# Optimization experiments

Hardware: AMD Instinct MI355X
Metric: run time of the kernel (lower is better)

## Reference

```python
import jax, jax.numpy as jnp
import numpy as np

B = 2048; SQ = 64; PC = 24; F = 16; H = 128; D = 256; T = 128; A = 4672
NSQ = B * SQ; NPC = B * PC


def setup_inputs() -> dict:
    key = jax.random.key(0)
    ks = iter(jax.random.split(key, 48))
    def nrm(shape, s=0.05):
        return jax.random.normal(next(ks), shape, dtype=jnp.float32) * s
    def edges(e_per, src_per, dst_per):
        # per-graph local edges: graph_offset + local node index
        g = jnp.repeat(jnp.arange(B), e_per)
        src = g * src_per + jax.random.randint(next(ks), (B * e_per,), 0, src_per)
        dst = g * dst_per + jax.random.randint(next(ks), (B * e_per,), 0, dst_per)
        return jnp.stack([src, dst]).astype(jnp.int32)
    gp = jnp.repeat(jnp.arange(B), PC)
    occ_src = jnp.arange(NPC, dtype=jnp.int32)                       # each piece occupies one square
    occ_dst = (gp * SQ + jax.random.randint(next(ks), (NPC,), 0, SQ)).astype(jnp.int32)
    ei_occ = jnp.stack([occ_src, occ_dst])                           # piece -> square
    ei_rev = ei_occ[::-1]                                            # square -> piece (rev_occupied_by)
    return dict(
        x_sq=jax.random.normal(next(ks), (NSQ, F), dtype=jnp.float32),
        x_pc=jax.random.normal(next(ks), (NPC, F), dtype=jnp.float32),
        W_in_sq=nrm((F, H)), b_in_sq=jnp.zeros((H,), jnp.float32),
        W_in_pc=nrm((F, H)), b_in_pc=jnp.zeros((H,), jnp.float32),
        W_adj=nrm((H, H)), W_occ=nrm((H, H)), W_att=nrm((H, H)), W_def=nrm((H, H)), W_rev=nrm((H, H)),
        W_out=nrm((H, D)), b_out=jnp.zeros((D,), jnp.float32),
        W_pt=nrm((D, T)), b_pt=jnp.zeros((T,), jnp.float32),
        W_vt=nrm((D, T)), b_vt=jnp.zeros((T,), jnp.float32),
        W_ph=nrm((T, A)), b_ph=jnp.zeros((A,), jnp.float32),
        W_vh=nrm((T, 1)), b_vh=jnp.zeros((1,), jnp.float32),
        ei_adj=edges(420, SQ, SQ),
        ei_occ=ei_occ,
        ei_att=edges(40, PC, PC),
        ei_def=edges(40, PC, PC),
        ei_rev=ei_rev,
        square_batch=jnp.repeat(jnp.arange(B), SQ).astype(jnp.int32),
        piece_batch=gp.astype(jnp.int32),
    )


def reference(x_sq, x_pc, W_in_sq, b_in_sq, W_in_pc, b_in_pc,
              W_adj, W_occ, W_att, W_def, W_rev, W_out, b_out,
              W_pt, b_pt, W_vt, b_vt, W_ph, b_ph, W_vh, b_vh,
              ei_adj, ei_occ, ei_att, ei_def, ei_rev, square_batch, piece_batch):
    gelu = jax.nn.gelu
    seg = jax.ops.segment_sum
    # per-node-type input encoders
    h_sq = gelu(x_sq @ W_in_sq + b_in_sq)          # [NSQ, H]
    h_pc = gelu(x_pc @ W_in_pc + b_in_pc)          # [NPC, H]
    # heterogeneous message passing: gather -> linear -> scatter-sum per edge type
    agg_sq = seg(h_sq[ei_adj[0]] @ W_adj, ei_adj[1], NSQ)
    agg_sq = agg_sq + seg(h_pc[ei_occ[0]] @ W_occ, ei_occ[1], NSQ)
    agg_pc = seg(h_pc[ei_att[0]] @ W_att, ei_att[1], NPC)
    agg_pc = agg_pc + seg(h_pc[ei_def[0]] @ W_def, ei_def[1], NPC)
    agg_pc = agg_pc + seg(h_sq[ei_rev[0]] @ W_rev, ei_rev[1], NPC)
    h_sq2 = gelu(h_sq + agg_sq)
    h_pc2 = gelu(h_pc + agg_pc)
    # project to embed_dim and mean-pool per graph
    out_sq = gelu(h_sq2 @ W_out + b_out)           # [NSQ, D]
    out_pc = gelu(h_pc2 @ W_out + b_out)           # [NPC, D]
    shared = seg(out_sq, square_batch, B) / SQ + seg(out_pc, piece_batch, B) / PC  # [B, D]
    # dual trunks + heads (exactly as in ChessNetwork.forward)
    policy_logits = gelu(shared @ W_pt + b_pt) @ W_ph + b_ph        # [B, 4672]
    value = jnp.tanh(gelu(shared @ W_vt + b_vt) @ W_vh + b_vh)      # [B, 1]
    return policy_logits, value
```

## Files before the change

kernel.cpp:

```cpp
#include <hip/hip_runtime.h>

#define BATCH 2048
#define SQN 64
#define PCN 24
#define FEAT 16
#define HID 128
#define DOUT 256
#define TDIM 128
#define ADIM 4672
#define NSQT (BATCH*SQN)
#define NPCT (BATCH*PCN)
#define E_ADJ 420
#define E_ATT 40
#define E_ADJ_TOT (BATCH*E_ADJ)
#define E_ATT_TOT (BATCH*E_ATT)

typedef unsigned short u16;
typedef unsigned int u32;
typedef __attribute__((ext_vector_type(8))) short bf16x8;
typedef __attribute__((ext_vector_type(8))) unsigned short u16x8;
typedef __attribute__((ext_vector_type(4))) float f32x4;
typedef __attribute__((ext_vector_type(2))) unsigned int u32x2;
typedef __attribute__((ext_vector_type(4))) unsigned int u32x4;

#define OFF_WADJ_H 0
#define OFF_WADJ_L 16384
#define OFF_WOCC_H 32768
#define OFF_WOCC_L 49152
#define OFF_WATT_H 65536
#define OFF_WATT_L 81920
#define OFF_WDEF_H 98304
#define OFF_WDEF_L 114688
#define OFF_WREV_H 131072
#define OFF_WREV_L 147456
#define OFF_WOUT_H 163840
#define OFF_WOUT_L 196608
#define OFF_WPH_H  229376
#define OFF_WPH_L  827392
#define OFF_WINSQ_H 1425408
#define OFF_WINSQ_L 1429504
#define OFF_WINPC_H 1433600
#define OFF_WINPC_L 1437696
#define WB_TOTAL    1441792

#define K_SMEM 81920

#define PHP_OFF  0
#define PAH_OFF  24576
#define PAL_OFF  36864
#define PEA_OFF  49152
#define PED_OFF  49472
#define PSA_OFF  49792
#define PSD_OFF  50112
#define PRSA_OFF 50432
#define PCUA_OFF 50692
#define PCNA_OFF 50948
#define PRSD_OFF 51204
#define PCUD_OFF 51464
#define PCND_OFF 51720
#define PRVS_OFF 51976
#define PRVD_OFF 52168

__device__ __forceinline__ u32 cvtpk(float a, float b) {
    u32 r;
    asm("v_cvt_pk_bf16_f32 %0, %1, %2" : "=v"(r) : "v"(a), "v"(b));
    return r;
}
__device__ __forceinline__ u16 f2b(float x) { return (u16)cvtpk(x, x); }
__device__ __forceinline__ float b2f(u16 h) { return __uint_as_float(((u32)h) << 16); }
__device__ __forceinline__ void split2(float x, u16& h, u16& l) {
    u32 wp = cvtpk(x, x);
    h = (u16)wp;
    float r = x - __uint_as_float(wp << 16);
    l = (u16)cvtpk(r, r);
}
__device__ __forceinline__ void split_pk(float a, float b, u32& wh, u32& wl) {
    wh = cvtpk(a, b);
    float ra = a - __uint_as_float(wh << 16);
    float rb = b - __uint_as_float(wh & 0xffff0000u);
    wl = cvtpk(ra, rb);
}
__device__ __forceinline__ float gelu_f(float x) {
    float x2 = x * x;
    float z2 = x * __builtin_fmaf(x2, 0.0713548162f, 1.5957691216f);
    float e = __expf(z2);
    return x - x * __fdividef(1.0f, e + 1.0f);
}
__device__ __forceinline__ f32x4 MFMA(bf16x8 a, bf16x8 b, f32x4 c) {
    return __builtin_amdgcn_mfma_f32_16x16x32_bf16(a, b, c, 0, 0, 0);
}
__device__ __forceinline__ bf16x8 bzero() {
    bf16x8 v = {0,0,0,0,0,0,0,0}; return v;
}
__device__ __forceinline__ void xfrag(const float* __restrict__ xrow, int g,
                                      bf16x8& ah, bf16x8& al)
{
    const f32x4 a = *(const f32x4*)(xrow + g*8);
    const f32x4 b = *(const f32x4*)(xrow + g*8 + 4);
    u32 h0,h1,h2,h3,l0,l1,l2,l3;
    split_pk(a[0], a[1], h0, l0);
    split_pk(a[2], a[3], h1, l1);
    split_pk(b[0], b[1], h2, l2);
    split_pk(b[2], b[3], h3, l3);
    u32x4 vh = {h0,h1,h2,h3};
    u32x4 vl = {l0,l1,l2,l3};
    ah = *(bf16x8*)&vh;
    al = *(bf16x8*)&vl;
}

template<int NT, int RT>
__device__ __forceinline__ void gemm_nt(
    const unsigned char* Ah, const unsigned char* Al,
    const u16* __restrict__ wh, const u16* __restrict__ wl,
    int ntBase, int lane, int g, int lr, f32x4 (&c)[NT][RT])
{
    const int sw = lr << 4;
    #pragma unroll
    for (int ks = 0; ks < 4; ++ks) {
        const int ko = ks*64 + g*16;
        bf16x8 ah[RT], al[RT];
        #pragma unroll
        for (int rt = 0; rt < RT; ++rt) {
            const int ro = (rt*16 + lr)*256 + (ko ^ sw);
            ah[rt] = *(const bf16x8*)(Ah + ro);
            al[rt] = *(const bf16x8*)(Al + ro);
        }
        #pragma unroll
        for (int ntl = 0; ntl < NT; ++ntl) {
            bf16x8 bh = *(const bf16x8*)(wh + (((ntBase+ntl)*4 + ks)*64 + lane)*8);
            bf16x8 bl = *(const bf16x8*)(wl + (((ntBase+ntl)*4 + ks)*64 + lane)*8);
            #pragma unroll
            for (int rt = 0; rt < RT; ++rt) {
                c[ntl][rt] = MFMA(ah[rt], bh, c[ntl][rt]);
                c[ntl][rt] = MFMA(al[rt], bh, c[ntl][rt]);
                c[ntl][rt] = MFMA(ah[rt], bl, c[ntl][rt]);
            }
        }
    }
}

__device__ __forceinline__ void gather_f32_8(
    const unsigned char* H, const int* srt, int st, int en, int cq8, float (&acc)[16])
{
    for (int i = st; i < en; ++i) {
        const int s = srt[i];
        const unsigned char* rp = H + s*512;
        const int sw2 = (s & 15) << 4;
        #pragma unroll
        for (int u = 0; u < 4; ++u) {
            f32x4 v = *(const f32x4*)(rp + ((cq8*64 + u*16) ^ sw2));
            acc[u*4+0] += v[0]; acc[u*4+1] += v[1];
            acc[u*4+2] += v[2]; acc[u*4+3] += v[3];
        }
    }
}
__device__ __forceinline__ void writeA_8(
    unsigned char* Ah, unsigned char* Al, int d, int cq8, const float (&acc)[16])
{
    unsigned char* wh = Ah + d*256;
    unsigned char* wl = Al + d*256;
    const int dw = (d & 15) << 4;
    #pragma unroll
    for (int u = 0; u < 2; ++u) {
        u32 oh[4], ol[4];
        #pragma unroll
        for (int j = 0; j < 4; ++j)
            split_pk(acc[u*8 + j*2], acc[u*8 + j*2 + 1], oh[j], ol[j]);
        u32x4 vh = {oh[0], oh[1], oh[2], oh[3]};
        u32x4 vl = {ol[0], ol[1], ol[2], ol[3]};
        *(u32x4*)(wh + ((cq8*32 + u*16) ^ dw)) = vh;
        *(u32x4*)(wl + ((cq8*32 + u*16) ^ dw)) = vl;
    }
}

__global__ __launch_bounds__(256) void k_prep(
    const float* __restrict__ W_adj, const float* __restrict__ W_occ,
    const float* __restrict__ W_att, const float* __restrict__ W_def,
    const float* __restrict__ W_rev, const float* __restrict__ W_out,
    const float* __restrict__ W_ph,
    const float* __restrict__ W_in_sq, const float* __restrict__ W_in_pc,
    u16* __restrict__ wb)
{
    int gid = blockIdx.x*256 + threadIdx.x;
    int fid = gid >> 6, lane = gid & 63;
    int g8 = (lane >> 4) * 8, lr = lane & 15;
    u16x8 vh, vl;
    if (fid >= 1392) {
        int f = fid - 1392;
        const float* src = (f < 8) ? W_in_sq : W_in_pc;
        int oh = (f < 8) ? OFF_WINSQ_H : OFF_WINPC_H;
        int ol = (f < 8) ? OFF_WINSQ_L : OFF_WINPC_L;
        int nt = f & 7;
        int col = nt*16 + lr;
        #pragma unroll
        for (int j = 0; j < 8; ++j) {
            int k = g8 + j;
            float v = (k < 16) ? src[k*HID + col] : 0.f;
            u16 h, l; split2(v, h, l);
            vh[j] = h; vl[j] = l;
        }
        *(u16x8*)(wb + oh + (nt*64 + lane)*8) = vh;
        *(u16x8*)(wb + ol + (nt*64 + lane)*8) = vl;
        return;
    }
    const float* src; int ld, f, oh, ol;
    if (fid < 32)       { src = W_adj; ld = HID;  f = fid;      oh = OFF_WADJ_H; ol = OFF_WADJ_L; }
    else if (fid < 64)  { src = W_occ; ld = HID;  f = fid-32;   oh = OFF_WOCC_H; ol = OFF_WOCC_L; }
    else if (fid < 96)  { src = W_att; ld = HID;  f = fid-64;   oh = OFF_WATT_H; ol = OFF_WATT_L; }
    else if (fid < 128) { src = W_def; ld = HID;  f = fid-96;   oh = OFF_WDEF_H; ol = OFF_WDEF_L; }
    else if (fid < 160) { src = W_rev; ld = HID;  f = fid-128;  oh = OFF_WREV_H; ol = OFF_WREV_L; }
    else if (fid < 224) { src = W_out; ld = DOUT; f = fid-160;  oh = OFF_WOUT_H; ol = OFF_WOUT_L; }
    else                { src = W_ph;  ld = ADIM; f = fid-224;  oh = OFF_WPH_H;  ol = OFF_WPH_L; }
    int nt = f >> 2, kb = f & 3;
    int col = nt*16 + lr;
    #pragma unroll
    for (int j = 0; j < 8; ++j) {
        int k = kb*32 + g8 + j;
        u16 h, l; split2(src[k*ld + col], h, l);
        vh[j] = h; vl[j] = l;
    }
    *(u16x8*)(wb + oh + (f*64 + lane)*8) = vh;
    *(u16x8*)(wb + ol + (f*64 + lane)*8) = vl;
}

__device__ __forceinline__ void sq_path(
    unsigned char* SMb, int b, int t,
    const float* __restrict__ x_sq, const float* __restrict__ x_pc,
    const float* __restrict__ b_in_sq, const float* __restrict__ b_in_pc,
    const float* __restrict__ b_out,
    const int* __restrict__ ei_adj, const int* __restrict__ ei_occ,
    const u16* __restrict__ wb, float* __restrict__ shared_sq)
{
    unsigned char* Hs_h  = SMb;
    unsigned char* Hs_l  = SMb + 16384;
    int*           Mint  = (int*)(SMb + 32768);
    unsigned char* HOT_h = SMb + 32768;
    unsigned char* HOT_l = SMb + 40960;
    unsigned char* Mocc  = SMb + 49152;
    unsigned char* A_h   = SMb + 32768;
    unsigned char* A_l   = SMb + 49152;
    unsigned char* Madj  = SMb + 65536;
    unsigned char* Hp    = SMb + 73728;

    const int w = t >> 6, lane = t & 63, g = lane >> 4, lr = lane & 15;
    const int colp = w*16 + lr;

    #pragma unroll
    for (int i = 0; i < 8; ++i) Mint[t + i*512] = 0;
    ((u32*)Mocc)[t] = 0;
    ((u32*)Mocc)[t + 512] = 0;
    ((u32*)(Hp + 6144))[t] = 0;
    __syncthreads();

    for (int i = t; i < E_ADJ; i += 512) {
        int s = ei_adj[b*E_ADJ + i] - b*SQN;
        int d = ei_adj[E_ADJ_TOT + b*E_ADJ + i] - b*SQN;
        atomicAdd(&Mint[d*64 + s], 1);
    }
    if (t < PCN) {
        int p = ei_occ[b*PCN + t] - b*PCN;
        int d = ei_occ[NPCT + b*PCN + t] - b*SQN;
        *(u16*)(Mocc + d*64 + ((p*2) ^ ((d&3)<<4))) = 0x3F80;
    }
    __syncthreads();

    #pragma unroll
    for (int ii = 0; ii < 4; ++ii) {
        int i = t + ii*512;
        int row = i >> 5, cp = i & 31;
        float v0 = (float)Mint[row*64 + cp*2];
        float v1 = (float)Mint[row*64 + cp*2 + 1];
        *(u32*)(Madj + row*128 + ((cp*4) ^ ((row&7)<<4))) = cvtpk(v0, v1);
    }
    float hv[16];
    {
        const f32x4 z = {0.f,0.f,0.f,0.f};
        f32x4 ch[4] = {z,z,z,z};
        {
            bf16x8 bh = *(const bf16x8*)(wb + OFF_WINSQ_H + (w*64 + lane)*8);
            bf16x8 bl = *(const bf16x8*)(wb + OFF_WINSQ_L + (w*64 + lane)*8);
            #pragma unroll
            for (int rt = 0; rt < 4; ++rt) {
                bf16x8 ah = bzero(), al = bzero();
                if (g < 2) xfrag(x_sq + (b*SQN + rt*16 + lr)*FEAT, g, ah, al);
                ch[rt] = MFMA(ah, bh, ch[rt]);
                ch[rt] = MFMA(al, bh, ch[rt]);
                ch[rt] = MFMA(ah, bl, ch[rt]);
            }
        }
        const float bbs = b_in_sq[colp];
        #pragma unroll
        for (int rt = 0; rt < 4; ++rt)
            #pragma unroll
            for (int r = 0; r < 4; ++r) {
                const int row = rt*16 + g*4 + r;
                float h = gelu_f(ch[rt][r] + bbs);
                hv[rt*4 + r] = h;
                u16 hh, ll; split2(h, hh, ll);
                const int bo = row*256 + ((colp*2) ^ ((row&15)<<4));
                *(u16*)(Hs_h + bo) = hh;
                *(u16*)(Hs_l + bo) = ll;
            }
        f32x4 cp2[2] = {z, z};
        {
            bf16x8 bh = *(const bf16x8*)(wb + OFF_WINPC_H + (w*64 + lane)*8);
            bf16x8 bl = *(const bf16x8*)(wb + OFF_WINPC_L + (w*64 + lane)*8);
            #pragma unroll
            for (int rt = 0; rt < 2; ++rt) {
                const int row = rt*16 + lr;
                bf16x8 ah = bzero(), al = bzero();
                if (g < 2 && row < PCN) xfrag(x_pc + (b*PCN + row)*FEAT, g, ah, al);
                cp2[rt] = MFMA(ah, bh, cp2[rt]);
                cp2[rt] = MFMA(al, bh, cp2[rt]);
                cp2[rt] = MFMA(ah, bl, cp2[rt]);
            }
        }
        const float bbp = b_in_pc[colp];
        #pragma unroll
        for (int rt = 0; rt < 2; ++rt)
            #pragma unroll
            for (int r = 0; r < 4; ++r) {
                const int row = rt*16 + g*4 + r;
                if (row < PCN) {
                    float h = gelu_f(cp2[rt][r] + bbp);
                    *(u16*)(Hp + row*256 + ((colp*2) ^ ((row&15)<<4))) = f2b(h);
                }
            }
    }
    __syncthreads();

    f32x4 hwj[4], hwo[2];
    {
        const f32x4 z = {0.f,0.f,0.f,0.f};
        hwj[0]=z; hwj[1]=z; hwj[2]=z; hwj[3]=z; hwo[0]=z; hwo[1]=z;
        const int sw15 = lr << 4;
        #pragma unroll
        for (int ks = 0; ks < 4; ++ks) {
            const int ko = ks*64 + g*16;
            bf16x8 bh = *(const bf16x8*)(wb + OFF_WADJ_H + ((w*4 + ks)*64 + lane)*8);
            bf16x8 bl = *(const bf16x8*)(wb + OFF_WADJ_L + ((w*4 + ks)*64 + lane)*8);
            #pragma unroll
            for (int rt = 0; rt < 4; ++rt) {
                const int ro = (rt*16 + lr)*256 + (ko ^ sw15);
                bf16x8 ah = *(const bf16x8*)(Hs_h + ro);
                bf16x8 al = *(const bf16x8*)(Hs_l + ro);
                hwj[rt] = MFMA(ah, bh, hwj[rt]);
                hwj[rt] = MFMA(al, bh, hwj[rt]);
                hwj[rt] = MFMA(ah, bl, hwj[rt]);
            }
            bf16x8 oh = *(const bf16x8*)(wb + OFF_WOCC_H + ((w*4 + ks)*64 + lane)*8);
            bf16x8 ol = *(const bf16x8*)(wb + OFF_WOCC_L + ((w*4 + ks)*64 + lane)*8);
            #pragma unroll
            for (int rt = 0; rt < 2; ++rt) {
                const int ro = (rt*16 + lr)*256 + (ko ^ sw15);
                bf16x8 ah = *(const bf16x8*)(Hp + ro);
                hwo[rt] = MFMA(ah, oh, hwo[rt]);
                hwo[rt] = MFMA(ah, ol, hwo[rt]);
            }
        }
    }
    __syncthreads();

    {
        const int swj = (lr & 7) << 4;
        #pragma unroll
        for (int rt = 0; rt < 4; ++rt) {
            u32 h01, l01, h23, l23;
            split_pk(hwj[rt][0], hwj[rt][1], h01, l01);
            split_pk(hwj[rt][2], hwj[rt][3], h23, l23);
            const int off = colp*128 + ((rt*32 + g*8) ^ swj);
            *(u32x2*)(Hs_h + off) = (u32x2){h01, h23};
            *(u32x2*)(Hs_l + off) = (u32x2){l01, l23};
        }
        const int swo = (lr & 3) << 4;
        #pragma unroll
        for (int rt = 0; rt < 2; ++rt) {
            u32 h01, l01, h23, l23;
            split_pk(hwo[rt][0], hwo[rt][1], h01, l01);
            split_pk(hwo[rt][2], hwo[rt][3], h23, l23);
            const int off = colp*64 + ((rt*32 + g*8) ^ swo);
            *(u32x2*)(HOT_h + off) = (u32x2){h01, h23};
            *(u32x2*)(HOT_l + off) = (u32x2){l01, l23};
        }
    }
    __syncthreads();

    f32x4 c1[4];
    {
        const f32x4 z = {0.f,0.f,0.f,0.f};
        c1[0]=z; c1[1]=z; c1[2]=z; c1[3]=z;
        const int swj = (lr & 7) << 4;
        #pragma unroll
        for (int ks = 0; ks < 2; ++ks) {
            const int bo = colp*128 + ((ks*64 + g*16) ^ swj);
            bf16x8 bh = *(const bf16x8*)(Hs_h + bo);
            bf16x8 bl = *(const bf16x8*)(Hs_l + bo);
            #pragma unroll
            for (int rt = 0; rt < 4; ++rt) {
                const int ao = (rt*16 + lr)*128 + ((ks*64 + g*16) ^ swj);
                bf16x8 am = *(const bf16x8*)(Madj + ao);
                c1[rt] = MFMA(am, bh, c1[rt]);
                c1[rt] = MFMA(am, bl, c1[rt]);
            }
        }
        const int swo = (lr & 3) << 4;
        {
            const int bo = colp*64 + ((g*16) ^ swo);
            bf16x8 bh = *(const bf16x8*)(HOT_h + bo);
            bf16x8 bl = *(const bf16x8*)(HOT_l + bo);
            #pragma unroll
            for (int rt = 0; rt < 4; ++rt) {
                const int ao = (rt*16 + lr)*64 + ((g*16) ^ swo);
                bf16x8 am = *(const bf16x8*)(Mocc + ao);
                c1[rt] = MFMA(am, bh, c1[rt]);
                c1[rt] = MFMA(am, bl, c1[rt]);
            }
        }
    }
    __syncthreads();

    #pragma unroll
    for (int rt = 0; rt < 4; ++rt)
        #pragma unroll
        for (int r = 0; r < 4; ++r) {
            const int row = rt*16 + g*4 + r;
            float h2 = gelu_f(c1[rt][r] + hv[rt*4 + r]);
            u16 hh, ll; split2(h2, hh, ll);
            const int bo = row*256 + ((colp*2) ^ ((row&15)<<4));
            *(u16*)(A_h + bo) = hh;
            *(u16*)(A_l + bo) = ll;
        }
    __syncthreads();

    f32x4 c2[2][4];
    {
        const f32x4 z = {0.f,0.f,0.f,0.f};
        #pragma unroll
        for (int n = 0; n < 2; ++n)
            #pragma unroll
            for (int rt = 0; rt < 4; ++rt) c2[n][rt] = z;
    }
    gemm_nt<2,4>(A_h, A_l, wb + OFF_WOUT_H, wb + OFF_WOUT_L, w*2, lane, g, lr, c2);
    #pragma unroll
    for (int ntl = 0; ntl < 2; ++ntl) {
        const int col = (w*2 + ntl)*16 + lr;
        const float bias = b_out[col];
        float cs = 0.f;
        #pragma unroll
        for (int rt = 0; rt < 4; ++rt)
            #pragma unroll
            for (int r = 0; r < 4; ++r) cs += gelu_f(c2[ntl][rt][r] + bias);
        cs += __shfl_xor(cs, 16);
        cs += __shfl_xor(cs, 32);
        if (lane < 16) shared_sq[b*DOUT + col] = cs * (1.0f/64.0f);
    }
}

__device__ __forceinline__ void pc_path(
    unsigned char* SMb, int pcb, int t,
    const float* __restrict__ x_sq, const float* __restrict__ x_pc,
    const float* __restrict__ b_in_sq, const float* __restrict__ b_in_pc,
    const float* __restrict__ b_out,
    const int* __restrict__ ei_att, const int* __restrict__ ei_def,
    const int* __restrict__ ei_rev,
    const u16* __restrict__ wb, float* __restrict__ shared_pc)
{
    unsigned char* Hp = SMb + PHP_OFF;
    unsigned char* Ah = SMb + PAH_OFF;
    unsigned char* Al = SMb + PAL_OFF;
    int* ea_pk = (int*)(SMb + PEA_OFF);
    int* ed_pk = (int*)(SMb + PED_OFF);
    int* srt_a = (int*)(SMb + PSA_OFF);
    int* srt_d = (int*)(SMb + PSD_OFF);
    int* rs_a  = (int*)(SMb + PRSA_OFF);
    int* cur_a = (int*)(SMb + PCUA_OFF);
    int* cnt_a = (int*)(SMb + PCNA_OFF);
    int* rs_d  = (int*)(SMb + PRSD_OFF);
    int* cur_d = (int*)(SMb + PCUD_OFF);
    int* cnt_d = (int*)(SMb + PCND_OFF);
    int* rv_s  = (int*)(SMb + PRVS_OFF);
    int* rv_d  = (int*)(SMb + PRVD_OFF);

    const int w = t >> 6, lane = t & 63, g = lane >> 4, lr = lane & 15;
    const int NR = 2*PCN;

    for (int i = t; i < 2*E_ATT; i += 512) {
        int sb = (i >= E_ATT) ? 1 : 0;
        int e = i - sb*E_ATT;
        int gb = pcb*2 + sb;
        int ro = sb*PCN - gb*PCN;
        int s = ei_att[gb*E_ATT + e] + ro;
        int d = ei_att[E_ATT_TOT + gb*E_ATT + e] + ro;
        ea_pk[i] = s | (d << 16);
        s = ei_def[gb*E_ATT + e] + ro;
        d = ei_def[E_ATT_TOT + gb*E_ATT + e] + ro;
        ed_pk[i] = s | (d << 16);
    }
    if (t < NR) {
        int sb = (t >= PCN) ? 1 : 0;
        int gb = pcb*2 + sb;
        int p = t - sb*PCN;
        rv_s[t] = ei_rev[gb*PCN + p];
        rv_d[t] = ei_rev[NPCT + gb*PCN + p] - gb*PCN + sb*PCN;
    }
    if (t < 64) { cnt_a[t] = 0; cnt_d[t] = 0; }
    __syncthreads();

    for (int i = t; i < 2*E_ATT; i += 512) {
        atomicAdd(&cnt_a[ea_pk[i] >> 16], 1);
        atomicAdd(&cnt_d[ed_pk[i] >> 16], 1);
    }
    __syncthreads();

    if (t < 64) {
        int v = cnt_a[t], o0 = v;
        for (int o = 1; o < 64; o <<= 1) { int u = __shfl_up(v, o); if (t >= o) v += u; }
        rs_a[t+1] = v; cur_a[t] = v - o0; if (t == 0) rs_a[0] = 0;
    } else if (t < 128) {
        int l = t - 64;
        int v = cnt_d[l], o0 = v;
        for (int o = 1; o < 64; o <<= 1) { int u = __shfl_up(v, o); if (l >= o) v += u; }
        rs_d[l+1] = v; cur_d[l] = v - o0; if (l == 0) rs_d[0] = 0;
    }
    __syncthreads();

    for (int i = t; i < 2*E_ATT; i += 512) {
        int pk = ea_pk[i];
        int p = atomicAdd(&cur_a[pk >> 16], 1); srt_a[p] = pk & 0xffff;
        pk = ed_pk[i];
        p = atomicAdd(&cur_d[pk >> 16], 1); srt_d[p] = pk & 0xffff;
    }
    {
        const int colp = w*16 + lr;
        const f32x4 z = {0.f,0.f,0.f,0.f};
        f32x4 cp[3] = {z,z,z};
        {
            bf16x8 bh = *(const bf16x8*)(wb + OFF_WINPC_H + (w*64 + lane)*8);
            bf16x8 bl = *(const bf16x8*)(wb + OFF_WINPC_L + (w*64 + lane)*8);
            #pragma unroll
            for (int rt = 0; rt < 3; ++rt) {
                bf16x8 ah = bzero(), al = bzero();
                if (g < 2) xfrag(x_pc + (pcb*NR + rt*16 + lr)*FEAT, g, ah, al);
                cp[rt] = MFMA(ah, bh, cp[rt]);
                cp[rt] = MFMA(al, bh, cp[rt]);
                cp[rt] = MFMA(ah, bl, cp[rt]);
            }
        }
        const float bbp = b_in_pc[colp];
        #pragma unroll
        for (int rt = 0; rt < 3; ++rt)
            #pragma unroll
            for (int r = 0; r < 4; ++r) {
                const int row = rt*16 + g*4 + r;
                float h = gelu_f(cp[rt][r] + bbp);
                *(float*)(Hp + row*512 + ((colp*4) ^ ((row&15)<<4))) = h;
            }
        f32x4 cr[3] = {z,z,z};
        {
            bf16x8 bh = *(const bf16x8*)(wb + OFF_WINSQ_H + (w*64 + lane)*8);
            bf16x8 bl = *(const bf16x8*)(wb + OFF_WINSQ_L + (w*64 + lane)*8);
            #pragma unroll
            for (int rt = 0; rt < 3; ++rt) {
                bf16x8 ah = bzero(), al = bzero();
                if (g < 2) {
                    int gr = rv_s[rt*16 + lr];
                    xfrag(x_sq + gr*FEAT, g, ah, al);
                }
                cr[rt] = MFMA(ah, bh, cr[rt]);
                cr[rt] = MFMA(al, bh, cr[rt]);
                cr[rt] = MFMA(ah, bl, cr[rt]);
            }
        }
        const float bbs = b_in_sq[colp];
        #pragma unroll
        for (int rt = 0; rt < 3; ++rt)
            #pragma unroll
            for (int r = 0; r < 4; ++r) {
                const int row0 = rt*16 + g*4 + r;
                const int dr = rv_d[row0];
                float h = gelu_f(cr[rt][r] + bbs);
                u16 hh, ll; split2(h, hh, ll);
                const int bo = dr*256 + ((colp*2) ^ ((dr&15)<<4));
                *(u16*)(Ah + bo) = hh;
                *(u16*)(Al + bo) = ll;
            }
    }
    __syncthreads();

    f32x4 c1[1][3];
    {
        const f32x4 z = {0.f,0.f,0.f,0.f};
        #pragma unroll
        for (int rt = 0; rt < 3; ++rt) c1[0][rt] = z;
    }
    gemm_nt<1,3>(Ah, Al, wb + OFF_WREV_H, wb + OFF_WREV_L, w, lane, g, lr, c1);
    __syncthreads();

    {
        const int d = t >> 3, cq8 = t & 7;
        if (d < NR) {
            float acc[16];
            #pragma unroll
            for (int i = 0; i < 16; ++i) acc[i] = 0.f;
            gather_f32_8(Hp, srt_a, rs_a[d], rs_a[d+1], cq8, acc);
            writeA_8(Ah, Al, d, cq8, acc);
        }
    }
    __syncthreads();

    gemm_nt<1,3>(Ah, Al, wb + OFF_WATT_H, wb + OFF_WATT_L, w, lane, g, lr, c1);
    __syncthreads();

    {
        const int d = t >> 3, cq8 = t & 7;
        if (d < NR) {
            float acc[16];
            #pragma unroll
            for (int i = 0; i < 16; ++i) acc[i] = 0.f;
            gather_f32_8(Hp, srt_d, rs_d[d], rs_d[d+1], cq8, acc);
            writeA_8(Ah, Al, d, cq8, acc);
        }
    }
    __syncthreads();

    gemm_nt<1,3>(Ah, Al, wb + OFF_WDEF_H, wb + OFF_WDEF_L, w, lane, g, lr, c1);
    __syncthreads();

    {
        const int colp = w*16 + lr;
        #pragma unroll
        for (int rt = 0; rt < 3; ++rt)
            #pragma unroll
            for (int r = 0; r < 4; ++r) {
                const int row = rt*16 + g*4 + r;
                float hvv = *(const float*)(Hp + row*512 + ((colp*4) ^ ((row&15)<<4)));
                float h2 = gelu_f(c1[0][rt][r] + hvv);
                u16 hh, ll; split2(h2, hh, ll);
                const int bo = row*256 + ((colp*2) ^ ((row&15)<<4));
                *(u16*)(Ah + bo) = hh;
                *(u16*)(Al + bo) = ll;
            }
    }
    __syncthreads();

    f32x4 c2[2][3];
    {
        const f32x4 z = {0.f,0.f,0.f,0.f};
        #pragma unroll
        for (int n = 0; n < 2; ++n)
            #pragma unroll
            for (int rt = 0; rt < 3; ++rt) c2[n][rt] = z;
    }
    gemm_nt<2,3>(Ah, Al, wb + OFF_WOUT_H, wb + OFF_WOUT_L, w*2, lane, g, lr, c2);
    #pragma unroll
    for (int ntl = 0; ntl < 2; ++ntl) {
        const int col = (w*2 + ntl)*16 + lr;
        const float bias = b_out[col];
        float s0 = 0.f, s1 = 0.f;
        #pragma unroll
        for (int r = 0; r < 4; ++r) s0 += gelu_f(c2[ntl][0][r] + bias);
        {
            float tt = 0.f;
            #pragma unroll
            for (int r = 0; r < 4; ++r) tt += gelu_f(c2[ntl][1][r] + bias);
            s0 += (g < 2) ? tt : 0.f;
            s1 += (g < 2) ? 0.f : tt;
        }
        #pragma unroll
        for (int r = 0; r < 4; ++r) s1 += gelu_f(c2[ntl][2][r] + bias);
        s0 += __shfl_xor(s0, 16); s0 += __shfl_xor(s0, 32);
        s1 += __shfl_xor(s1, 16); s1 += __shfl_xor(s1, 32);
        if (lane < 16) {
            const int b0 = pcb*2, b1 = b0 + 1;
            shared_pc[b0*DOUT + col] = s0 * (1.0f/PCN);
            shared_pc[b1*DOUT + col] = s1 * (1.0f/PCN);
        }
    }
}

__global__ __launch_bounds__(512, 4) void k_main(
    const float* __restrict__ x_sq, const float* __restrict__ x_pc,
    const float* __restrict__ b_in_sq, const float* __restrict__ b_in_pc,
    const float* __restrict__ b_out,
    const int* __restrict__ ei_adj, const int* __restrict__ ei_occ,
    const int* __restrict__ ei_att, const int* __restrict__ ei_def,
    const int* __restrict__ ei_rev,
    const u16* __restrict__ wb,
    float* __restrict__ shared_sq, float* __restrict__ shared_pc)
{
    extern __shared__ __align__(16) unsigned char SMb[];
    const int bid = blockIdx.x;
    const int grp = bid / 3, rem = bid - grp*3;
    if (rem < 2) {
        sq_path(SMb, grp*2 + rem, threadIdx.x, x_sq, x_pc, b_in_sq, b_in_pc,
                b_out, ei_adj, ei_occ, wb, shared_sq);
    } else {
        pc_path(SMb, grp, threadIdx.x, x_sq, x_pc, b_in_sq, b_in_pc,
                b_out, ei_att, ei_def, ei_rev, wb, shared_pc);
    }
}

__global__ __launch_bounds__(256) void k_head(
    const float* __restrict__ shared_sq, const float* __restrict__ shared_pc,
    const float* __restrict__ W_pt, const float* __restrict__ b_pt,
    const float* __restrict__ W_vt, const float* __restrict__ b_vt,
    const float* __restrict__ W_vh, const float* __restrict__ b_vh,
    u16* __restrict__ tpol_h, u16* __restrict__ tpol_l, float* __restrict__ out_value)
{
    __shared__ float sh[2*DOUT];
    __shared__ float vred[2*TDIM];
    const int t = threadIdx.x;
    const int hh = t >> 7, j = t & 127;
    const int b = blockIdx.x*2 + hh;
    for (int i = t; i < 2*DOUT; i += 256)
        sh[i] = shared_sq[blockIdx.x*2*DOUT + i] + shared_pc[blockIdx.x*2*DOUT + i];
    __syncthreads();
    const float* s = sh + hh*DOUT;
    float ap = b_pt[j], av = b_vt[j];
    #pragma unroll 8
    for (int k = 0; k < DOUT; ++k) {
        float sv = s[k];
        ap += sv * W_pt[k*TDIM + j];
        av += sv * W_vt[k*TDIM + j];
    }
    float tv = gelu_f(ap);
    u16 th, tl; split2(tv, th, tl);
    tpol_h[b*TDIM + j] = th;
    tpol_l[b*TDIM + j] = tl;
    vred[hh*TDIM + j] = gelu_f(av) * W_vh[j];
    __syncthreads();
    for (int stp = 64; stp > 0; stp >>= 1) {
        if (j < stp) vred[hh*TDIM + j] += vred[hh*TDIM + j + stp];
        __syncthreads();
    }
    if (j == 0) out_value[b] = tanhf(vred[hh*TDIM] + b_vh[0]);
}

__global__ __launch_bounds__(256) void k_pol(
    const u16* __restrict__ tpol_h, const u16* __restrict__ tpol_l,
    const u16* __restrict__ wb, const float* __restrict__ b_ph,
    float* __restrict__ pol)
{
    const u16* wph_h = wb + OFF_WPH_H;
    const u16* wph_l = wb + OFF_WPH_L;
    const int t = threadIdx.x, w = t >> 6, lane = t & 63, g = lane >> 4, lr = lane & 15;
    const int nt = blockIdx.x*4 + w;
    const int rbase = blockIdx.y*64;
    f32x4 acc[4];
    const f32x4 z = {0.f,0.f,0.f,0.f};
    #pragma unroll
    for (int rt = 0; rt < 4; ++rt) acc[rt] = z;
    #pragma unroll
    for (int ks = 0; ks < 4; ++ks) {
        bf16x8 bh = *(const bf16x8*)(wph_h + ((nt*4 + ks)*64 + lane)*8);
        bf16x8 bl = *(const bf16x8*)(wph_l + ((nt*4 + ks)*64 + lane)*8);
        #pragma unroll
        for (int rt = 0; rt < 4; ++rt) {
            const int ro = (rbase + rt*16 + lr)*TDIM + ks*32 + g*8;
            bf16x8 ah = *(const bf16x8*)(tpol_h + ro);
            bf16x8 al = *(const bf16x8*)(tpol_l + ro);
            acc[rt] = MFMA(ah, bh, acc[rt]);
            acc[rt] = MFMA(al, bh, acc[rt]);
            acc[rt] = MFMA(ah, bl, acc[rt]);
        }
    }
    const float bias = b_ph[nt*16 + lr];
    #pragma unroll
    for (int rt = 0; rt < 4; ++rt)
        #pragma unroll
        for (int r = 0; r < 4; ++r) {
            int row = rbase + rt*16 + g*4 + r;
            pol[(size_t)row*ADIM + nt*16 + lr] = acc[rt][r] + bias;
        }
}

extern "C" void kernel_launch(void* const* d_in, const int* in_sizes, int n_in,
                              void* d_out, int out_size, void* d_ws, size_t ws_size,
                              hipStream_t stream) {
    (void)in_sizes; (void)n_in; (void)out_size; (void)ws_size;
    const float* x_sq    = (const float*)d_in[0];
    const float* x_pc    = (const float*)d_in[1];
    const float* W_in_sq = (const float*)d_in[2];
    const float* b_in_sq = (const float*)d_in[3];
    const float* W_in_pc = (const float*)d_in[4];
    const float* b_in_pc = (const float*)d_in[5];
    const float* W_adj   = (const float*)d_in[6];
    const float* W_occ   = (const float*)d_in[7];
    const float* W_att   = (const float*)d_in[8];
    const float* W_def   = (const float*)d_in[9];
    const float* W_rev   = (const float*)d_in[10];
    const float* W_out   = (const float*)d_in[11];
    const float* b_out   = (const float*)d_in[12];
    const float* W_pt    = (const float*)d_in[13];
    const float* b_pt    = (const float*)d_in[14];
    const float* W_vt    = (const float*)d_in[15];
    const float* b_vt    = (const float*)d_in[16];
    const float* W_ph    = (const float*)d_in[17];
    const float* b_ph    = (const float*)d_in[18];
    const float* W_vh    = (const float*)d_in[19];
    const float* b_vh    = (const float*)d_in[20];
    const int* ei_adj    = (const int*)d_in[21];
    const int* ei_occ    = (const int*)d_in[22];
    const int* ei_att    = (const int*)d_in[23];
    const int* ei_def    = (const int*)d_in[24];
    const int* ei_rev    = (const int*)d_in[25];

    float* out = (float*)d_out;
    float* pol = out;
    float* val = out + (size_t)BATCH * ADIM;

    float* shared_sq = (float*)d_ws;
    float* shared_pc = shared_sq + BATCH*DOUT;
    u16* tpol_h = (u16*)(shared_pc + BATCH*DOUT);
    u16* tpol_l = tpol_h + BATCH*TDIM;
    u16* wb     = tpol_l + BATCH*TDIM;

    hipFuncSetAttribute((const void*)k_main,
                        hipFuncAttributeMaxDynamicSharedMemorySize, K_SMEM);

    k_prep<<<352, 256, 0, stream>>>(W_adj, W_occ, W_att, W_def, W_rev, W_out, W_ph,
                                    W_in_sq, W_in_pc, wb);
    k_main<<<3072, 512, K_SMEM, stream>>>(x_sq, x_pc, b_in_sq, b_in_pc, b_out,
                                          ei_adj, ei_occ, ei_att, ei_def, ei_rev,
                                          wb, shared_sq, shared_pc);
    k_head<<<BATCH/2, 256, 0, stream>>>(shared_sq, shared_pc, W_pt, b_pt, W_vt, b_vt,
                                        W_vh, b_vh, tpol_h, tpol_l, val);
    k_pol<<<dim3(ADIM/64, BATCH/64), 256, 0, stream>>>(tpol_h, tpol_l, wb, b_ph, pol);
}
```

Measured before the change: 198.2 us.

## Move trunk head GEMMs onto MFMA with pre-split bf16 weights

The policy/value trunk projection (shared @ W_pt, shared @ W_vt) now runs on MFMA matrix cores using a three-term bf16 hi/lo split, with W_pt and W_vt pre-packed in k_prep. k_head switches from 1024 scalar-FMA blocks to 64 blocks of 512 threads, each covering 32 rows, and reduces the value head with wave shuffles. Separately, the A-fragment loads in gemm_nt are moved inside the inner loop to cut register pressure. The head now has few blocks, which may underuse the GPU, and the three-term split keeps precision close to fp32.

New measurement: 187.7 us. 1.06x faster.

```diff
diff --git a/kernel.cpp b/kernel.cpp
--- a/kernel.cpp
+++ b/kernel.cpp
@@ -41,7 +41,11 @@
 #define OFF_WINSQ_L 1429504
 #define OFF_WINPC_H 1433600
 #define OFF_WINPC_L 1437696
-#define WB_TOTAL    1441792
+#define OFF_WPT_H  1441792
+#define OFF_WPT_L  1474560
+#define OFF_WVT_H  1507328
+#define OFF_WVT_L  1540096
+#define WB_TOTAL   1572864
 
 #define K_SMEM 81920
 
@@ -117,23 +121,19 @@
     const int sw = lr << 4;
     #pragma unroll
     for (int ks = 0; ks < 4; ++ks) {
-        const int ko = ks*64 + g*16;
-        bf16x8 ah[RT], al[RT];
-        #pragma unroll
-        for (int rt = 0; rt < RT; ++rt) {
-            const int ro = (rt*16 + lr)*256 + (ko ^ sw);
-            ah[rt] = *(const bf16x8*)(Ah + ro);
-            al[rt] = *(const bf16x8*)(Al + ro);
-        }
+        const int ko = (ks*64 + g*16) ^ sw;
         #pragma unroll
         for (int ntl = 0; ntl < NT; ++ntl) {
             bf16x8 bh = *(const bf16x8*)(wh + (((ntBase+ntl)*4 + ks)*64 + lane)*8);
             bf16x8 bl = *(const bf16x8*)(wl + (((ntBase+ntl)*4 + ks)*64 + lane)*8);
             #pragma unroll
             for (int rt = 0; rt < RT; ++rt) {
-                c[ntl][rt] = MFMA(ah[rt], bh, c[ntl][rt]);
-                c[ntl][rt] = MFMA(al[rt], bh, c[ntl][rt]);
-                c[ntl][rt] = MFMA(ah[rt], bl, c[ntl][rt]);
+                const int ro = (rt*16 + lr)*256 + ko;
+                bf16x8 ah = *(const bf16x8*)(Ah + ro);
+                bf16x8 al = *(const bf16x8*)(Al + ro);
+                c[ntl][rt] = MFMA(ah, bh, c[ntl][rt]);
+                c[ntl][rt] = MFMA(al, bh, c[ntl][rt]);
+                c[ntl][rt] = MFMA(ah, bl, c[ntl][rt]);
             }
         }
     }
@@ -179,12 +179,31 @@
     const float* __restrict__ W_rev, const float* __restrict__ W_out,
     const float* __restrict__ W_ph,
     const float* __restrict__ W_in_sq, const float* __restrict__ W_in_pc,
+    const float* __restrict__ W_pt, const float* __restrict__ W_vt,
     u16* __restrict__ wb)
 {
     int gid = blockIdx.x*256 + threadIdx.x;
     int fid = gid >> 6, lane = gid & 63;
     int g8 = (lane >> 4) * 8, lr = lane & 15;
     u16x8 vh, vl;
+    if (fid >= 1408) {
+        int f = fid - 1408;
+        int which = f >> 6, f2 = f & 63;
+        const float* src = which ? W_vt : W_pt;
+        int oh = which ? OFF_WVT_H : OFF_WPT_H;
+        int ol = which ? OFF_WVT_L : OFF_WPT_L;
+        int nt = f2 >> 3, kb = f2 & 7;
+        int col = nt*16 + lr;
+        #pragma unroll
+        for (int j = 0; j < 8; ++j) {
+            int k = kb*32 + g8 + j;
+            u16 h, l; split2(src[k*TDIM + col], h, l);
+            vh[j] = h; vl[j] = l;
+        }
+        *(u16x8*)(wb + oh + (f2*64 + lane)*8) = vh;
+        *(u16x8*)(wb + ol + (f2*64 + lane)*8) = vl;
+        return;
+    }
     if (fid >= 1392) {
         int f = fid - 1392;
         const float* src = (f < 8) ? W_in_sq : W_in_pc;
@@ -336,12 +355,12 @@
         const int sw15 = lr << 4;
         #pragma unroll
         for (int ks = 0; ks < 4; ++ks) {
-            const int ko = ks*64 + g*16;
+            const int ko = (ks*64 + g*16) ^ sw15;
             bf16x8 bh = *(const bf16x8*)(wb + OFF_WADJ_H + ((w*4 + ks)*64 + lane)*8);
             bf16x8 bl = *(const bf16x8*)(wb + OFF_WADJ_L + ((w*4 + ks)*64 + lane)*8);
             #pragma unroll
             for (int rt = 0; rt < 4; ++rt) {
-                const int ro = (rt*16 + lr)*256 + (ko ^ sw15);
+                const int ro = (rt*16 + lr)*256 + ko;
                 bf16x8 ah = *(const bf16x8*)(Hs_h + ro);
                 bf16x8 al = *(const bf16x8*)(Hs_l + ro);
                 hwj[rt] = MFMA(ah, bh, hwj[rt]);
@@ -352,7 +371,7 @@
             bf16x8 ol = *(const bf16x8*)(wb + OFF_WOCC_L + ((w*4 + ks)*64 + lane)*8);
             #pragma unroll
             for (int rt = 0; rt < 2; ++rt) {
-                const int ro = (rt*16 + lr)*256 + (ko ^ sw15);
+                const int ro = (rt*16 + lr)*256 + ko;
                 bf16x8 ah = *(const bf16x8*)(Hp + ro);
                 hwo[rt] = MFMA(ah, oh, hwo[rt]);
                 hwo[rt] = MFMA(ah, ol, hwo[rt]);
@@ -530,6 +549,7 @@
         pk = ed_pk[i];
         p = atomicAdd(&cur_d[pk >> 16], 1); srt_d[p] = pk & 0xffff;
     }
+    float hv[8];
     {
         const int colp = w*16 + lr;
         const f32x4 z = {0.f,0.f,0.f,0.f};
@@ -700,40 +720,100 @@
     }
 }
 
-__global__ __launch_bounds__(256) void k_head(
+__global__ __launch_bounds__(512) void k_head(
     const float* __restrict__ shared_sq, const float* __restrict__ shared_pc,
-    const float* __restrict__ W_pt, const float* __restrict__ b_pt,
-    const float* __restrict__ W_vt, const float* __restrict__ b_vt,
+    const u16* __restrict__ wb,
+    const float* __restrict__ b_pt, const float* __restrict__ b_vt,
     const float* __restrict__ W_vh, const float* __restrict__ b_vh,
     u16* __restrict__ tpol_h, u16* __restrict__ tpol_l, float* __restrict__ out_value)
 {
-    __shared__ float sh[2*DOUT];
-    __shared__ float vred[2*TDIM];
+    __shared__ __align__(16) unsigned char SH[33792];
+    unsigned char* Ah = SH;
+    unsigned char* Al = SH + 16384;
+    float* vpart = (float*)(SH + 32768);
+
     const int t = threadIdx.x;
-    const int hh = t >> 7, j = t & 127;
-    const int b = blockIdx.x*2 + hh;
-    for (int i = t; i < 2*DOUT; i += 256)
-        sh[i] = shared_sq[blockIdx.x*2*DOUT + i] + shared_pc[blockIdx.x*2*DOUT + i];
-    __syncthreads();
-    const float* s = sh + hh*DOUT;
-    float ap = b_pt[j], av = b_vt[j];
-    #pragma unroll 8
-    for (int k = 0; k < DOUT; ++k) {
-        float sv = s[k];
-        ap += sv * W_pt[k*TDIM + j];
-        av += sv * W_vt[k*TDIM + j];
-    }
-    float tv = gelu_f(ap);
-    u16 th, tl; split2(tv, th, tl);
-    tpol_h[b*TDIM + j] = th;
-    tpol_l[b*TDIM + j] = tl;
-    vred[hh*TDIM + j] = gelu_f(av) * W_vh[j];
-    __syncthreads();
-    for (int stp = 64; stp > 0; stp >>= 1) {
-        if (j < stp) vred[hh*TDIM + j] += vred[hh*TDIM + j + stp];
-        __syncthreads();
-    }
-    if (j == 0) out_value[b] = tanhf(vred[hh*TDIM] + b_vh[0]);
+    const int w = t >> 6, lane = t & 63, g = lane >> 4, lr = lane & 15;
+    const int rbase = blockIdx.x * 32;
+
+    {
+        const int row = t >> 4, c0 = (t & 15) * 16;
+        const float* s1 = shared_sq + (size_t)(rbase + row)*DOUT + c0;
+        const float* s2 = shared_pc + (size_t)(rbase + row)*DOUT + c0;
+        const int sw = (row & 15) << 4;
+        #pragma unroll
+        for (int cc = 0; cc < 2; ++cc) {
+            f32x4 a = *(const f32x4*)(s1 + cc*8);
+            f32x4 b = *(const f32x4*)(s2 + cc*8);
+            f32x4 a2 = *(const f32x4*)(s1 + cc*8 + 4);
+            f32x4 b2 = *(const f32x4*)(s2 + cc*8 + 4);
+            float v0=a[0]+b[0], v1=a[1]+b[1], v2=a[2]+b[2], v3=a[3]+b[3];
+            float v4=a2[0]+b2[0], v5=a2[1]+b2[1], v6=a2[2]+b2[2], v7=a2[3]+b2[3];
+            u32 h0,h1,h2,h3,l0,l1,l2,l3;
+            split_pk(v0,v1,h0,l0); split_pk(v2,v3,h1,l1);
+            split_pk(v4,v5,h2,l2); split_pk(v6,v7,h3,l3);
+            u32x4 vh = {h0,h1,h2,h3};
+            u32x4 vl = {l0,l1,l2,l3};
+            *(u32x4*)(Ah + row*512 + ((c0*2 + cc*16) ^ sw)) = vh;
+            *(u32x4*)(Al + row*512 + ((c0*2 + cc*16) ^ sw)) = vl;
+        }
+    }
+    __syncthreads();
+
+    f32x4 cpt[2], cvt[2];
+    {
+        const f32x4 z = {0.f,0.f,0.f,0.f};
+        cpt[0]=z; cpt[1]=z; cvt[0]=z; cvt[1]=z;
+        const int sw = lr << 4;
+        #pragma unroll
+        for (int ks = 0; ks < 8; ++ks) {
+            const int ko = (ks*64 + g*16) ^ sw;
+            bf16x8 ph_ = *(const bf16x8*)(wb + OFF_WPT_H + ((w*8 + ks)*64 + lane)*8);
+            bf16x8 pl_ = *(const bf16x8*)(wb + OFF_WPT_L + ((w*8 + ks)*64 + lane)*8);
+            bf16x8 vh_ = *(const bf16x8*)(wb + OFF_WVT_H + ((w*8 + ks)*64 + lane)*8);
+            bf16x8 vl_ = *(const bf16x8*)(wb + OFF_WVT_L + ((w*8 + ks)*64 + lane)*8);
+            #pragma unroll
+            for (int rt = 0; rt < 2; ++rt) {
+                const int ao = (rt*16 + lr)*512 + ko;
+                bf16x8 ah = *(const bf16x8*)(Ah + ao);
+                bf16x8 al = *(const bf16x8*)(Al + ao);
+                cpt[rt] = MFMA(ah, ph_, cpt[rt]);
+                cpt[rt] = MFMA(al, ph_, cpt[rt]);
+                cpt[rt] = MFMA(ah, pl_, cpt[rt]);
+                cvt[rt] = MFMA(ah, vh_, cvt[rt]);
+                cvt[rt] = MFMA(al, vh_, cvt[rt]);
+                cvt[rt] = MFMA(ah, vl_, cvt[rt]);
+            }
+        }
+    }
+
+    {
+        const int col = w*16 + lr;
+        const float bpt = b_pt[col], bvt = b_vt[col], wvh = W_vh[col];
+        #pragma unroll
+        for (int rt = 0; rt < 2; ++rt)
+            #pragma unroll
+            for (int r = 0; r < 4; ++r) {
+                const int row = rt*16 + g*4 + r;
+                float tv = gelu_f(cpt[rt][r] + bpt);
+                u16 th, tl; split2(tv, th, tl);
+                tpol_h[(size_t)(rbase + row)*TDIM + col] = th;
+                tpol_l[(size_t)(rbase + row)*TDIM + col] = tl;
+                float vv = gelu_f(cvt[rt][r] + bvt) * wvh;
+                vv += __shfl_xor(vv, 1);
+                vv += __shfl_xor(vv, 2);
+                vv += __shfl_xor(vv, 4);
+                vv += __shfl_xor(vv, 8);
+                if (lr == 0) vpart[row*8 + w] = vv;
+            }
+    }
+    __syncthreads();
+    if (t < 32) {
+        float s = 0.f;
+        #pragma unroll
+        for (int j = 0; j < 8; ++j) s += vpart[t*8 + j];
+        out_value[rbase + t] = tanhf(s + b_vh[0]);
+    }
 }
 
 __global__ __launch_bounds__(256) void k_pol(
@@ -818,12 +898,12 @@
     hipFuncSetAttribute((const void*)k_main,
                         hipFuncAttributeMaxDynamicSharedMemorySize, K_SMEM);
 
-    k_prep<<<352, 256, 0, stream>>>(W_adj, W_occ, W_att, W_def, W_rev, W_out, W_ph,
-                                    W_in_sq, W_in_pc, wb);
+    k_prep<<<384, 256, 0, stream>>>(W_adj, W_occ, W_att, W_def, W_rev, W_out, W_ph,
+                                    W_in_sq, W_in_pc, W_pt, W_vt, wb);
     k_main<<<3072, 512, K_SMEM, stream>>>(x_sq, x_pc, b_in_sq, b_in_pc, b_out,
                                           ei_adj, ei_occ, ei_att, ei_def, ei_rev,
                                           wb, shared_sq, shared_pc);
-    k_head<<<BATCH/2, 256, 0, stream>>>(shared_sq, shared_pc, W_pt, b_pt, W_vt, b_vt,
-                                        W_vh, b_vh, tpol_h, tpol_l, val);
+    k_head<<<64, 512, 0, stream>>>(shared_sq, shared_pc, wb, b_pt, b_vt, W_vh, b_vh,
+                                   tpol_h, tpol_l, val);
     k_pol<<<dim3(ADIM/64, BATCH/64), 256, 0, stream>>>(tpol_h, tpol_l, wb, b_ph, pol);
 }
```
